# Optimization experiments

Measured on AMD Instinct MI355X. Metric: run time of the kernel, lower is better.

The kernel has to match this reference:

```python
import jax, jax.numpy as jnp
import numpy as np

B, S, D = 2, 2048, 1024
H = 16
DH = D // H  # 64


def setup_inputs() -> dict:
    key = jax.random.key(0)
    k1, k2, k3 = jax.random.split(key, 3)
    x = jax.random.normal(k1, (B, S, D), dtype=jnp.float32)
    W_qkv = jax.random.normal(k2, (D, 3 * D), dtype=jnp.float32) * 0.01
    b_qkv = jnp.zeros((3 * D,), dtype=jnp.float32)
    W_out = jax.random.normal(k3, (D, D), dtype=jnp.float32) * 0.01
    b_out = jnp.zeros((D,), dtype=jnp.float32)
    return {"x": x, "W_qkv": W_qkv, "b_qkv": b_qkv, "W_out": W_out, "b_out": b_out}


def reference(x, W_qkv, b_qkv, W_out, b_out):
    b, s, d = x.shape
    h, dh = H, DH
    # fused QKV projection
    qkv = x @ W_qkv + b_qkv                       # [b, s, 3d]
    qkv = qkv.reshape(b, s, 3, h, dh)
    q, k, v = qkv[:, :, 0], qkv[:, :, 1], qkv[:, :, 2]  # [b, s, h, dh]
    q = q.transpose(0, 2, 1, 3)                    # [b, h, s, dh]
    k = k.transpose(0, 2, 1, 3)
    v = v.transpose(0, 2, 1, 3)
    inv_sqrt_d = jnp.asarray(1.0 / np.sqrt(dh), dtype=x.dtype)
    scores = jnp.einsum('bhqd,bhkd->bhqk', q, k) * inv_sqrt_d  # [b, h, s, s]
    causal = jnp.tril(jnp.ones((s, s), dtype=bool))[None, None]
    # source masks with -10000.0 (not -inf)
    scores = jnp.where(causal, scores, jnp.asarray(-10000.0, dtype=scores.dtype))
    probs = jax.nn.softmax(scores, axis=-1)
    attn = jnp.einsum('bhqk,bhkd->bhqd', probs, v)  # [b, h, s, dh]
    attn = attn.transpose(0, 2, 1, 3).reshape(b, s, d)
    return attn @ W_out + b_out
```

## Files before the change

kernel.cpp:

```cpp
#include <hip/hip_runtime.h>
#include <hip/hip_bf16.h>

#define B_  2
#define S_  2048
#define D_  1024
#define H_  16
#define DH_ 64
#define M_  (B_ * S_)
#define QKV_LD (3 * D_)

typedef __bf16 bf16x8 __attribute__((ext_vector_type(8)));
typedef float  f32x4  __attribute__((ext_vector_type(4)));
typedef unsigned short us4 __attribute__((ext_vector_type(4)));
typedef unsigned short us8 __attribute__((ext_vector_type(8)));

__device__ inline unsigned short f2bf(float f) {
  union { __bf16 h; unsigned short u; } cv; cv.h = (__bf16)f; return cv.u;
}
__device__ inline float bf2f(unsigned short u) {
  union { unsigned int i; float f; } cv; cv.i = ((unsigned int)u) << 16; return cv.f;
}
__device__ inline unsigned int pk2bf(float lo, float hi) {
  return (unsigned int)f2bf(lo) | ((unsigned int)f2bf(hi) << 16);
}
__device__ inline void cstore(float* p, float v) { *p = v; }
__device__ inline void cstore(unsigned short* p, float v) { *p = f2bf(v); }

__device__ inline void gload_lds16(const void* g, void* lds) {
  __builtin_amdgcn_global_load_lds(
      (const __attribute__((address_space(1))) unsigned int*)g,
      (__attribute__((address_space(3))) unsigned int*)lds, 16, 0, 0);
}

__global__ __launch_bounds__(256) void prep_all(
    const float* __restrict__ x, unsigned short* __restrict__ x_bf,
    const float* __restrict__ W_qkv, unsigned short* __restrict__ wqkvT,
    const float* __restrict__ W_out, unsigned short* __restrict__ woutT) {
  __shared__ float tile[32][33];
  const int blk = blockIdx.x;
  const int t = threadIdx.x;
  if (blk < 4096) {
    int i = blk * 256 + t;
    float4 v = ((const float4*)x)[i];
    us4 p = { f2bf(v.x), f2bf(v.y), f2bf(v.z), f2bf(v.w) };
    ((us4*)x_bf)[i] = p;
    return;
  }
  const float* W; unsigned short* Wt; int K, N, bi;
  if (blk < 4096 + 3072) { bi = blk - 4096; W = W_qkv; Wt = wqkvT; K = D_; N = QKV_LD; }
  else                   { bi = blk - 7168; W = W_out; Wt = woutT; K = D_; N = D_; }
  const int bx = bi % (N / 32), by = bi / (N / 32);
  const int tx = t & 31, ty = t >> 5;
  const int c0 = bx * 32, r0 = by * 32;
  #pragma unroll
  for (int i = 0; i < 4; ++i)
    tile[ty + 8 * i][tx] = W[(size_t)(r0 + ty + 8 * i) * N + c0 + tx];
  __syncthreads();
  #pragma unroll
  for (int i = 0; i < 4; ++i)
    Wt[(size_t)(c0 + ty + 8 * i) * K + r0 + tx] = f2bf(tile[tx][ty + 8 * i]);
}

template<typename CT>
__global__ __launch_bounds__(256) void gemm_bf16_tn(
    const unsigned short* __restrict__ A,
    const unsigned short* __restrict__ Bt,
    const float* __restrict__ bias,
    CT* __restrict__ C, int N, int K) {
  __shared__ __align__(16) unsigned short smA[128 * 32];
  __shared__ __align__(16) unsigned short smB[128 * 32];
  const int t = threadIdx.x;
  const int w = t >> 6, l = t & 63;
  const int lg = l >> 4, lr = l & 15;
  const int row0 = blockIdx.y * 128, col0 = blockIdx.x * 128;
  const int wm = (w >> 1) * 64, wn = (w & 1) * 64;

  f32x4 acc[4][4] = {};

  for (int k0 = 0; k0 < K; k0 += 32) {
    __syncthreads();
    #pragma unroll
    for (int i = 0; i < 2; ++i) {
      const int inst = 2 * w + i;
      const int r = inst * 16 + (l >> 2);
      const int cb = (l & 3) * 8;
      gload_lds16(A  + (size_t)(row0 + r) * K + k0 + cb, &smA[inst * 512]);
      gload_lds16(Bt + (size_t)(col0 + r) * K + k0 + cb, &smB[inst * 512]);
    }
    __syncthreads();

    bf16x8 af[4], bfr[4];
    #pragma unroll
    for (int m = 0; m < 4; ++m)
      af[m] = *(const bf16x8*)&smA[(wm + m * 16 + lr) * 32 + lg * 8];
    #pragma unroll
    for (int n = 0; n < 4; ++n)
      bfr[n] = *(const bf16x8*)&smB[(wn + n * 16 + lr) * 32 + lg * 8];
    #pragma unroll
    for (int m = 0; m < 4; ++m)
      #pragma unroll
      for (int n = 0; n < 4; ++n)
        acc[m][n] = __builtin_amdgcn_mfma_f32_16x16x32_bf16(af[m], bfr[n], acc[m][n], 0, 0, 0);
  }

  #pragma unroll
  for (int m = 0; m < 4; ++m) {
    #pragma unroll
    for (int n = 0; n < 4; ++n) {
      const int col = col0 + wn + n * 16 + lr;
      const float bv = bias[col];
      #pragma unroll
      for (int r = 0; r < 4; ++r) {
        const int row = row0 + wm + m * 16 + lg * 4 + r;
        cstore(&C[(size_t)row * N + col], acc[m][n][r] + bv);
      }
    }
  }
}

__global__ __launch_bounds__(512, 4) void attn_fwd_mfma(
    const unsigned short* __restrict__ qkv, unsigned short* __restrict__ attn_out) {
  const int bid = blockIdx.x;
  const int xcd = bid & 7;
  const int li  = bid >> 3;
  const int bh  = xcd * 4 + (li >> 4);
  const int x   = li & 15;
  const int b = bh / H_, h = bh % H_;
  const unsigned short* base = qkv + (size_t)b * S_ * QKV_LD;

  __shared__ __align__(16) char smK[2][64 * 128];
  __shared__ __align__(16) char smV[2][64 * 128];

  const int t  = threadIdx.x;
  const int w  = t >> 6;
  const bool lo = (w < 4);
  const int wq = w & 3;
  const int l  = t & 63;
  const int lg = l >> 4;
  const int lr = l & 15;

  const int qt  = lo ? x : (31 - x);
  const int qw0 = qt * 64 + wq * 16;

  const unsigned short* kbase = base + D_ + h * DH_;
  const unsigned short* vbase = base + 2 * D_ + h * DH_;

  us8 kreg[2], vreg[2];
  const int kp  = (t & 31) * 2;
  const int vdb = ((t >> 5) & 7) * 8;

  auto issue_loads = [&](int k0) {
    #pragma unroll
    for (int it = 0; it < 2; ++it) {
      int idx = t + it * 256;
      int r = idx >> 3, c = idx & 7;
      kreg[it] = *(const us8*)(kbase + (size_t)(k0 + r) * QKV_LD + c * 8);
    }
    vreg[0] = *(const us8*)(vbase + (size_t)(k0 + kp) * QKV_LD + vdb);
    vreg[1] = *(const us8*)(vbase + (size_t)(k0 + kp + 1) * QKV_LD + vdb);
  };
  auto write_lds = [&](int buf) {
    #pragma unroll
    for (int it = 0; it < 2; ++it) {
      int idx = t + it * 256;
      int r = idx >> 3, c = idx & 7;
      int rho = (r & 0x23) | ((r & 0x04) << 2) | ((r & 0x18) >> 1);
      *(us8*)(smK[buf] + rho * 128 + ((c * 16) ^ ((rho & 7) << 4))) = kreg[it];
    }
    #pragma unroll
    for (int j = 0; j < 8; ++j) {
      int row = vdb + j;
      unsigned int pv = (unsigned int)vreg[0][j] | ((unsigned int)vreg[1][j] << 16);
      *(unsigned int*)(smV[buf] + row * 128 + ((2 * kp) ^ ((row & 7) << 4))) = pv;
    }
  };

  bf16x8 qf[2];
  {
    const unsigned short* qp = base + (size_t)(qw0 + lr) * QKV_LD + h * DH_ + 8 * lg;
    #pragma unroll
    for (int ks = 0; ks < 2; ++ks) {
      us8 qv = *(const us8*)(qp + 32 * ks);
      #pragma unroll
      for (int e = 0; e < 8; ++e) qf[ks][e] = (__bf16)(bf2f(qv[e]) * 0.18033688f);
    }
  }

  float mrun = -1e30f, lrun = 0.f;
  f32x4 acc_o[4] = {};

  const int ntiles = 32 - x;
  if (t < 256) { issue_loads(0); write_lds(0); }
  __syncthreads();

  for (int kti = 0; kti < ntiles; ++kti) {
    const int k0 = kti * 64;
    const int cur = kti & 1;

    if (t < 256 && kti + 1 < ntiles) issue_loads((kti + 1) * 64);

    const bool active = lo ? (kti <= x) : true;
    if (active) {
      f32x4 sc[4] = {};
      #pragma unroll
      for (int kt = 0; kt < 4; ++kt)
        #pragma unroll
        for (int ks = 0; ks < 2; ++ks) {
          int row = kt * 16 + lr;
          bf16x8 kb_ = *(const bf16x8*)(smK[cur] + row * 128 +
                                        (((ks * 64) + 16 * lg) ^ ((row & 7) << 4)));
          sc[kt] = __builtin_amdgcn_mfma_f32_16x16x32_bf16(kb_, qf[ks], sc[kt], 0, 0, 0);
        }

      if (k0 + 63 > qw0) {
        #pragma unroll
        for (int kt = 0; kt < 4; ++kt)
          #pragma unroll
          for (int r = 0; r < 4; ++r) {
            int kc = k0 + ((kt >> 1) << 5) + (lg << 3) + ((kt & 1) << 2) + r;
            if (kc > qw0 + lr) sc[kt][r] = -1e30f;
          }
      }

      float v = fmaxf(fmaxf(sc[0][0], sc[0][1]), fmaxf(sc[0][2], sc[0][3]));
      #pragma unroll
      for (int kt = 1; kt < 4; ++kt)
        v = fmaxf(v, fmaxf(fmaxf(sc[kt][0], sc[kt][1]), fmaxf(sc[kt][2], sc[kt][3])));
      v = fmaxf(v, __shfl_xor(v, 16));
      v = fmaxf(v, __shfl_xor(v, 32));
      if (!__all(v <= mrun + 8.0f)) {
        const float mnew = fmaxf(mrun, v);
        const float alpha = exp2f(mrun - mnew);
        mrun = mnew;
        float alphaO[4];
        #pragma unroll
        for (int r = 0; r < 4; ++r)
          alphaO[r] = __shfl(alpha, (l & 48) | (lg * 4 + r));
        #pragma unroll
        for (int dt = 0; dt < 4; ++dt)
          #pragma unroll
          for (int r = 0; r < 4; ++r) acc_o[dt][r] *= alphaO[r];
        lrun *= alpha;
      }
      float s = 0.f;
      #pragma unroll
      for (int kt = 0; kt < 4; ++kt)
        #pragma unroll
        for (int r = 0; r < 4; ++r) {
          float p = exp2f(sc[kt][r] - mrun);
          sc[kt][r] = p;
          s += p;
        }
      s += __shfl_xor(s, 16);
      s += __shfl_xor(s, 32);
      lrun += s;

      union { unsigned int u[4]; bf16x8 v8; } pa[2];
      #pragma unroll
      for (int ks = 0; ks < 2; ++ks) {
        pa[ks].u[0] = pk2bf(sc[2 * ks][0], sc[2 * ks][1]);
        pa[ks].u[1] = pk2bf(sc[2 * ks][2], sc[2 * ks][3]);
        pa[ks].u[2] = pk2bf(sc[2 * ks + 1][0], sc[2 * ks + 1][1]);
        pa[ks].u[3] = pk2bf(sc[2 * ks + 1][2], sc[2 * ks + 1][3]);
      }

      #pragma unroll
      for (int dt = 0; dt < 4; ++dt)
        #pragma unroll
        for (int ks = 0; ks < 2; ++ks) {
          int row = dt * 16 + lr;
          bf16x8 vb = *(const bf16x8*)(smV[cur] + row * 128 +
                                       (((ks * 64) + 16 * lg) ^ ((row & 7) << 4)));
          acc_o[dt] = __builtin_amdgcn_mfma_f32_16x16x32_bf16(pa[ks].v8, vb, acc_o[dt], 0, 0, 0);
        }
    }

    if (t < 256 && kti + 1 < ntiles) write_lds(cur ^ 1);
    __syncthreads();
  }

  const float inv = 1.0f / lrun;
  float invO[4];
  #pragma unroll
  for (int r = 0; r < 4; ++r)
    invO[r] = __shfl(inv, (l & 48) | (lg * 4 + r));
  #pragma unroll
  for (int dt = 0; dt < 4; ++dt)
    #pragma unroll
    for (int r = 0; r < 4; ++r)
      attn_out[(size_t)(b * S_ + qw0 + lg * 4 + r) * D_ + h * DH_ + dt * 16 + lr] =
          f2bf(acc_o[dt][r] * invO[r]);
}

extern "C" void kernel_launch(void* const* d_in, const int* in_sizes, int n_in,
                              void* d_out, int out_size, void* d_ws, size_t ws_size,
                              hipStream_t stream) {
  const float* x     = (const float*)d_in[0];
  const float* W_qkv = (const float*)d_in[1];
  const float* b_qkv = (const float*)d_in[2];
  const float* W_out = (const float*)d_in[3];
  const float* b_out = (const float*)d_in[4];
  float* out = (float*)d_out;

  char* ws = (char*)d_ws;
  unsigned short* qkv_bf  = (unsigned short*)ws;  ws += (size_t)M_ * QKV_LD * 2;
  unsigned short* attn_bf = (unsigned short*)ws;  ws += (size_t)M_ * D_ * 2;
  unsigned short* x_bf    = (unsigned short*)ws;  ws += (size_t)M_ * D_ * 2;
  unsigned short* wqkvT   = (unsigned short*)ws;  ws += (size_t)QKV_LD * D_ * 2;
  unsigned short* woutT   = (unsigned short*)ws;

  dim3 blk(256);
  prep_all<<<4096 + 3072 + 1024, blk, 0, stream>>>(x, x_bf, W_qkv, wqkvT, W_out, woutT);
  gemm_bf16_tn<unsigned short><<<dim3(QKV_LD / 128, M_ / 128), blk, 0, stream>>>(
      x_bf, wqkvT, b_qkv, qkv_bf, QKV_LD, D_);
  attn_fwd_mfma<<<dim3(512), dim3(512), 0, stream>>>(qkv_bf, attn_bf);
  gemm_bf16_tn<float><<<dim3(D_ / 128, M_ / 128), blk, 0, stream>>>(
      attn_bf, woutT, b_out, out, D_, D_);
}
```

Measured before the change: 121.8 us.

## Software-pipeline attention QK with softmax/PV and swizzle GEMM block order

The attention loop is restructured so the QK^T MFMAs for the next key tile run in the same step as softmax and PV for the current tile. K is prefetched two tiles ahead and V one tile ahead, and s_setprio raises wave priority around MFMA bursts. The aim is to overlap matrix-core work with the exp/shuffle softmax and global-load latency, at the cost of extra live score registers and more complex buffer indexing. The GEMM also remaps block IDs with an XCD-style swizzle so that neighbouring tiles share L2 cache.

```diff
diff --git a/kernel.cpp b/kernel.cpp
--- a/kernel.cpp
+++ b/kernel.cpp
@@ -72,7 +72,11 @@
   const int t = threadIdx.x;
   const int w = t >> 6, l = t & 63;
   const int lg = l >> 4, lr = l & 15;
-  const int row0 = blockIdx.y * 128, col0 = blockIdx.x * 128;
+  const int nwg  = gridDim.x * gridDim.y;
+  const int bid0 = blockIdx.y * gridDim.x + blockIdx.x;
+  const int swz  = (bid0 & 7) * (nwg >> 3) + (bid0 >> 3);
+  const int bx = swz % gridDim.x, by = swz / gridDim.x;
+  const int row0 = by * 128, col0 = bx * 128;
   const int wm = (w >> 1) * 64, wn = (w & 1) * 64;
 
   f32x4 acc[4][4] = {};
@@ -142,6 +146,9 @@
   const int qt  = lo ? x : (31 - x);
   const int qw0 = qt * 64 + wq * 16;
 
+  const int nt   = 32 - x;
+  const int myNT = lo ? (x + 1) : nt;
+
   const unsigned short* kbase = base + D_ + h * DH_;
   const unsigned short* vbase = base + 2 * D_ + h * DH_;
 
@@ -149,17 +156,21 @@
   const int kp  = (t & 31) * 2;
   const int vdb = ((t >> 5) & 7) * 8;
 
-  auto issue_loads = [&](int k0) {
+  auto issueK = [&](int tile) {
+    const int k0 = tile * 64;
     #pragma unroll
     for (int it = 0; it < 2; ++it) {
       int idx = t + it * 256;
       int r = idx >> 3, c = idx & 7;
       kreg[it] = *(const us8*)(kbase + (size_t)(k0 + r) * QKV_LD + c * 8);
     }
+  };
+  auto issueV = [&](int tile) {
+    const int k0 = tile * 64;
     vreg[0] = *(const us8*)(vbase + (size_t)(k0 + kp) * QKV_LD + vdb);
     vreg[1] = *(const us8*)(vbase + (size_t)(k0 + kp + 1) * QKV_LD + vdb);
   };
-  auto write_lds = [&](int buf) {
+  auto writeK = [&](int buf) {
     #pragma unroll
     for (int it = 0; it < 2; ++it) {
       int idx = t + it * 256;
@@ -167,6 +178,8 @@
       int rho = (r & 0x23) | ((r & 0x04) << 2) | ((r & 0x18) >> 1);
       *(us8*)(smK[buf] + rho * 128 + ((c * 16) ^ ((rho & 7) << 4))) = kreg[it];
     }
+  };
+  auto writeV = [&](int buf) {
     #pragma unroll
     for (int j = 0; j < 8; ++j) {
       int row = vdb + j;
@@ -189,95 +202,119 @@
   float mrun = -1e30f, lrun = 0.f;
   f32x4 acc_o[4] = {};
 
-  const int ntiles = 32 - x;
-  if (t < 256) { issue_loads(0); write_lds(0); }
-  __syncthreads();
-
-  for (int kti = 0; kti < ntiles; ++kti) {
-    const int k0 = kti * 64;
-    const int cur = kti & 1;
-
-    if (t < 256 && kti + 1 < ntiles) issue_loads((kti + 1) * 64);
-
-    const bool active = lo ? (kti <= x) : true;
-    if (active) {
-      f32x4 sc[4] = {};
-      #pragma unroll
-      for (int kt = 0; kt < 4; ++kt)
-        #pragma unroll
-        for (int ks = 0; ks < 2; ++ks) {
-          int row = kt * 16 + lr;
-          bf16x8 kb_ = *(const bf16x8*)(smK[cur] + row * 128 +
-                                        (((ks * 64) + 16 * lg) ^ ((row & 7) << 4)));
-          sc[kt] = __builtin_amdgcn_mfma_f32_16x16x32_bf16(kb_, qf[ks], sc[kt], 0, 0, 0);
-        }
-
-      if (k0 + 63 > qw0) {
-        #pragma unroll
-        for (int kt = 0; kt < 4; ++kt)
-          #pragma unroll
-          for (int r = 0; r < 4; ++r) {
-            int kc = k0 + ((kt >> 1) << 5) + (lg << 3) + ((kt & 1) << 2) + r;
-            if (kc > qw0 + lr) sc[kt][r] = -1e30f;
-          }
+  auto QK = [&](f32x4 (&sc)[4], int buf, int tile) {
+    const int k0 = tile * 64;
+    __builtin_amdgcn_s_setprio(1);
+    #pragma unroll
+    for (int kt = 0; kt < 4; ++kt) {
+      sc[kt] = f32x4{0.f, 0.f, 0.f, 0.f};
+      #pragma unroll
+      for (int ks = 0; ks < 2; ++ks) {
+        int row = kt * 16 + lr;
+        bf16x8 kb_ = *(const bf16x8*)(smK[buf] + row * 128 +
+                                      (((ks * 64) + 16 * lg) ^ ((row & 7) << 4)));
+        sc[kt] = __builtin_amdgcn_mfma_f32_16x16x32_bf16(kb_, qf[ks], sc[kt], 0, 0, 0);
       }
-
-      float v = fmaxf(fmaxf(sc[0][0], sc[0][1]), fmaxf(sc[0][2], sc[0][3]));
-      #pragma unroll
-      for (int kt = 1; kt < 4; ++kt)
-        v = fmaxf(v, fmaxf(fmaxf(sc[kt][0], sc[kt][1]), fmaxf(sc[kt][2], sc[kt][3])));
-      v = fmaxf(v, __shfl_xor(v, 16));
-      v = fmaxf(v, __shfl_xor(v, 32));
-      if (!__all(v <= mrun + 8.0f)) {
-        const float mnew = fmaxf(mrun, v);
-        const float alpha = exp2f(mrun - mnew);
-        mrun = mnew;
-        float alphaO[4];
-        #pragma unroll
-        for (int r = 0; r < 4; ++r)
-          alphaO[r] = __shfl(alpha, (l & 48) | (lg * 4 + r));
-        #pragma unroll
-        for (int dt = 0; dt < 4; ++dt)
-          #pragma unroll
-          for (int r = 0; r < 4; ++r) acc_o[dt][r] *= alphaO[r];
-        lrun *= alpha;
-      }
-      float s = 0.f;
+    }
+    __builtin_amdgcn_s_setprio(0);
+    if (k0 + 63 > qw0) {
       #pragma unroll
       for (int kt = 0; kt < 4; ++kt)
         #pragma unroll
         for (int r = 0; r < 4; ++r) {
-          float p = exp2f(sc[kt][r] - mrun);
-          sc[kt][r] = p;
-          s += p;
+          int kc = k0 + ((kt >> 1) << 5) + (lg << 3) + ((kt & 1) << 2) + r;
+          if (kc > qw0 + lr) sc[kt][r] = -1e30f;
         }
-      s += __shfl_xor(s, 16);
-      s += __shfl_xor(s, 32);
-      lrun += s;
-
-      union { unsigned int u[4]; bf16x8 v8; } pa[2];
-      #pragma unroll
-      for (int ks = 0; ks < 2; ++ks) {
-        pa[ks].u[0] = pk2bf(sc[2 * ks][0], sc[2 * ks][1]);
-        pa[ks].u[1] = pk2bf(sc[2 * ks][2], sc[2 * ks][3]);
-        pa[ks].u[2] = pk2bf(sc[2 * ks + 1][0], sc[2 * ks + 1][1]);
-        pa[ks].u[3] = pk2bf(sc[2 * ks + 1][2], sc[2 * ks + 1][3]);
-      }
-
+    }
+  };
+
+  auto SMPV = [&](f32x4 (&sc)[4], int buf) {
+    float v = fmaxf(fmaxf(sc[0][0], sc[0][1]), fmaxf(sc[0][2], sc[0][3]));
+    #pragma unroll
+    for (int kt = 1; kt < 4; ++kt)
+      v = fmaxf(v, fmaxf(fmaxf(sc[kt][0], sc[kt][1]), fmaxf(sc[kt][2], sc[kt][3])));
+    v = fmaxf(v, __shfl_xor(v, 16));
+    v = fmaxf(v, __shfl_xor(v, 32));
+    if (!__all(v <= mrun + 8.0f)) {
+      const float mnew = fmaxf(mrun, v);
+      const float alpha = exp2f(mrun - mnew);
+      mrun = mnew;
+      float alphaO[4];
+      #pragma unroll
+      for (int r = 0; r < 4; ++r)
+        alphaO[r] = __shfl(alpha, (l & 48) | (lg * 4 + r));
       #pragma unroll
       for (int dt = 0; dt < 4; ++dt)
         #pragma unroll
-        for (int ks = 0; ks < 2; ++ks) {
-          int row = dt * 16 + lr;
-          bf16x8 vb = *(const bf16x8*)(smV[cur] + row * 128 +
-                                       (((ks * 64) + 16 * lg) ^ ((row & 7) << 4)));
-          acc_o[dt] = __builtin_amdgcn_mfma_f32_16x16x32_bf16(pa[ks].v8, vb, acc_o[dt], 0, 0, 0);
-        }
-    }
-
-    if (t < 256 && kti + 1 < ntiles) write_lds(cur ^ 1);
-    __syncthreads();
-  }
+        for (int r = 0; r < 4; ++r) acc_o[dt][r] *= alphaO[r];
+      lrun *= alpha;
+    }
+    float s = 0.f;
+    #pragma unroll
+    for (int kt = 0; kt < 4; ++kt)
+      #pragma unroll
+      for (int r = 0; r < 4; ++r) {
+        float p = exp2f(sc[kt][r] - mrun);
+        sc[kt][r] = p;
+        s += p;
+      }
+    s += __shfl_xor(s, 16);
+    s += __shfl_xor(s, 32);
+    lrun += s;
+
+    union { unsigned int u[4]; bf16x8 v8; } pa[2];
+    #pragma unroll
+    for (int ks = 0; ks < 2; ++ks) {
+      pa[ks].u[0] = pk2bf(sc[2 * ks][0], sc[2 * ks][1]);
+      pa[ks].u[1] = pk2bf(sc[2 * ks][2], sc[2 * ks][3]);
+      pa[ks].u[2] = pk2bf(sc[2 * ks + 1][0], sc[2 * ks + 1][1]);
+      pa[ks].u[3] = pk2bf(sc[2 * ks + 1][2], sc[2 * ks + 1][3]);
+    }
+    __builtin_amdgcn_s_setprio(1);
+    #pragma unroll
+    for (int dt = 0; dt < 4; ++dt)
+      #pragma unroll
+      for (int ks = 0; ks < 2; ++ks) {
+        int row = dt * 16 + lr;
+        bf16x8 vb = *(const bf16x8*)(smV[buf] + row * 128 +
+                                     (((ks * 64) + 16 * lg) ^ ((row & 7) << 4)));
+        acc_o[dt] = __builtin_amdgcn_mfma_f32_16x16x32_bf16(pa[ks].v8, vb, acc_o[dt], 0, 0, 0);
+      }
+    __builtin_amdgcn_s_setprio(0);
+  };
+
+  if (t < 256) {
+    issueK(0); issueV(0);
+    writeK(0); writeV(0);
+    issueK(1); issueV(1);
+    writeK(1);
+    issueK(2);
+  }
+  __syncthreads();
+
+  f32x4 scA[4], scB[4];
+  QK(scA, 0, 0);
+  __syncthreads();
+
+  #define BODY(CONS, PROD, n)                                            \
+    {                                                                    \
+      const int cur = (n) & 1;                                           \
+      if (t < 256) {                                                     \
+        if ((n) + 2 < nt) writeK(cur);          \
+        if ((n) + 1 < nt) writeV(cur ^ 1);    \
+        if ((n) + 3 < nt) issueK((n) + 3);                               \
+        if ((n) + 2 < nt) issueV((n) + 2);                               \
+      }                                                                  \
+      if ((n) + 1 < myNT) QK(PROD, cur ^ 1, (n) + 1);                    \
+      if ((n) < myNT)     SMPV(CONS, cur);                               \
+      __syncthreads();                                                   \
+    }
+
+  for (int n = 0; n < nt; n += 2) {
+    BODY(scA, scB, n);
+    if (n + 1 < nt) BODY(scB, scA, n + 1);
+  }
+  #undef BODY
 
   const float inv = 1.0f / lrun;
   float invO[4];
```

After: 125.5 us. 1.03x slower.
